# Kernel tuning notes

Hardware: AMD Instinct MI355X
Metric: run time of the kernel (lower is better)

Reference implementation:

```python
import jax, jax.numpy as jnp
import numpy as np

THRESHOLDS = (0.3, 0.4, 0.5)
EPS_NORM = 1e-12   # F.normalize eps
EPS_MAX = 1e-5     # added to max before rescale


def setup_inputs() -> dict:
    key = jax.random.key(0)
    k1, k2 = jax.random.split(key)
    cam = jax.random.uniform(k1, (4, 64, 64), dtype=jnp.float32)
    feat = jax.random.normal(k2, (4, 256, 64, 64), dtype=jnp.float32)
    return {"cam": cam, "feat": feat}


def reference(cam, feat):
    # multi-threshold soft mask: mean of hard masks at each threshold -> (B,1,H,W)
    masks = jnp.stack([(cam >= t).astype(feat.dtype) for t in THRESHOLDS], axis=1)
    m = masks.mean(axis=1)[:, None]  # (B,1,H,W)
    masked = feat * m  # (B,C,H,W)

    B, C, H, W = masked.shape
    f = masked.reshape(B, C, H * W)  # (B,C,N)
    # L2-normalize over channel dim (torch F.normalize, dim=1)
    norm = jnp.sqrt(jnp.sum(f * f, axis=1, keepdims=True))
    fn = f / jnp.maximum(norm, EPS_NORM)

    # full pairwise similarity (B,N,N), then CAM-weighted aggregation
    sim = jnp.einsum('bcn,bcm->bnm', fn, fn)      # (B,N,N)
    camf = cam.reshape(B, H * W)                  # (B,N)
    out = jnp.einsum('bnm,bm->bn', sim, camf)     # (B,N)

    mn = out.min(axis=1, keepdims=True)
    mx = out.max(axis=1, keepdims=True) + EPS_MAX
    ref = ((out - mn) / (mx - mn)).reshape(B, H, W)

    loss = jnp.mean(jnp.abs(ref - jax.lax.stop_gradient(cam)))
    return ref, loss
```

## Files before the change

### kernel.cpp

```cpp
#include <hip/hip_runtime.h>


constexpr int B  = 4;
constexpr int C  = 256;
constexpr int N  = 4096;
constexpr int BN = B * N;
constexpr int CN = C * N;
constexpr int NBLK1 = 512;

__device__ __forceinline__ float wsum(float v) {
#pragma unroll
    for (int o = 32; o > 0; o >>= 1) v += __shfl_down(v, o, 64);
    return v;
}
__device__ __forceinline__ float wmin64(float v) {
#pragma unroll
    for (int o = 32; o > 0; o >>= 1) v = fminf(v, __shfl_down(v, o, 64));
    return v;
}
__device__ __forceinline__ float wmax64(float v) {
#pragma unroll
    for (int o = 32; o > 0; o >>= 1) v = fmaxf(v, __shfl_down(v, o, 64));
    return v;
}

__global__ void __launch_bounds__(256) k_norm_vpart(
    const float* __restrict__ cam, const float* __restrict__ feat,
    float* __restrict__ s, float* __restrict__ v_part,
    unsigned int* __restrict__ cnt)
{
    if (blockIdx.x == 0 && threadIdx.x == 0) *cnt = 0u;
    const int t   = threadIdx.x;
    const int pix = t & 31;
    const int g   = t >> 5;
    const int bk  = blockIdx.x;
    const int b   = bk >> 7;
    const int n0  = (bk * 32) & (N - 1);

    __shared__ float red[8][33];
    __shared__ float w_sh[32];

    {
        const float* fp = feat + (size_t)b * CN + (size_t)(g * 32) * N + n0 + pix;
        float ss = 0.f;
#pragma unroll 8
        for (int cc = 0; cc < 32; ++cc) {
            float x = fp[(size_t)cc * N];
            ss = fmaf(x, x, ss);
        }
        red[g][pix] = ss;
    }
    __syncthreads();
    if (t < 32) {
        float tot = 0.f;
#pragma unroll
        for (int gg = 0; gg < 8; ++gg) tot += red[gg][t];
        float cv = cam[bk * 32 + t];
        float m  = ((cv >= 0.3f ? 1.f : 0.f) + (cv >= 0.4f ? 1.f : 0.f) +
                    (cv >= 0.5f ? 1.f : 0.f)) * (1.f / 3.f);
        float norm = m * sqrtf(tot);
        float sc = m / fmaxf(norm, 1e-12f);
        s[bk * 32 + t] = sc;
        w_sh[t] = sc * cv;
    }
    __syncthreads();

    {
        const float* fp = feat + (size_t)b * CN + (size_t)t * N + n0;
        float acc = 0.f;
#pragma unroll
        for (int pp = 0; pp < 8; ++pp) {
            float4 x = *(const float4*)(fp + pp * 4);
            acc = fmaf(x.x, w_sh[pp * 4 + 0], acc);
            acc = fmaf(x.y, w_sh[pp * 4 + 1], acc);
            acc = fmaf(x.z, w_sh[pp * 4 + 2], acc);
            acc = fmaf(x.w, w_sh[pp * 4 + 3], acc);
        }
        v_part[bk * 256 + t] = acc;
    }
}

__global__ void __launch_bounds__(256) k_vreduce(
    const float* __restrict__ v_part, float* __restrict__ v)
{
    const int c = threadIdx.x;
    const int b = blockIdx.x;
    const float* base = v_part + (size_t)b * 128 * 256 + c;
    float acc = 0.f;
#pragma unroll 8
    for (int k = 0; k < 128; ++k) acc += base[k * 256];
    v[b * 256 + c] = acc;
}

__global__ void __launch_bounds__(256) k_out(
    const float* __restrict__ feat, const float* __restrict__ s,
    const float* __restrict__ v, float* __restrict__ ob,
    float* __restrict__ bmn, float* __restrict__ bmx)
{
    const int t   = threadIdx.x;
    const int pix = t & 31;
    const int g   = t >> 5;
    const int bk  = blockIdx.x;
    const int b   = bk >> 7;
    const int n0  = (bk * 32) & (N - 1);

    __shared__ float vs[C];
    vs[t] = v[b * C + t];
    __syncthreads();

    const float* fp = feat + (size_t)b * CN + (size_t)(g * 32) * N + n0 + pix;
    float acc = 0.f;
#pragma unroll 8
    for (int cc = 0; cc < 32; ++cc)
        acc = fmaf(fp[(size_t)cc * N], vs[g * 32 + cc], acc);

    __shared__ float red[8][33];
    red[g][pix] = acc;
    __syncthreads();
    if (t < 32) {
        float tot = 0.f;
#pragma unroll
        for (int gg = 0; gg < 8; ++gg) tot += red[gg][t];
        float o = s[bk * 32 + t] * tot;
        ob[bk * 32 + t] = o;
        float mn = o, mx = o;
#pragma unroll
        for (int o2 = 16; o2 > 0; o2 >>= 1) {
            mn = fminf(mn, __shfl_down(mn, o2, 64));
            mx = fmaxf(mx, __shfl_down(mx, o2, 64));
        }
        if (t == 0) { bmn[bk] = mn; bmx[bk] = mx; }
    }
}

__global__ void __launch_bounds__(256) k_final(
    const float* __restrict__ ob, const float* __restrict__ cam,
    const float* __restrict__ bmn, const float* __restrict__ bmx,
    float* __restrict__ out, float* __restrict__ part, unsigned int* __restrict__ cnt)
{
    const int t = threadIdx.x, blk = blockIdx.x;
    const int p = blk * 256 + t;
    const int b = blk >> 4;

    __shared__ float sh[2];
    if (t < 64) {
        float a = fminf(bmn[b * 128 + t], bmn[b * 128 + 64 + t]);
        a = wmin64(a);
        if (t == 0) sh[0] = a;
    } else if (t < 128) {
        int l = t - 64;
        float a = fmaxf(bmx[b * 128 + l], bmx[b * 128 + 64 + l]);
        a = wmax64(a);
        if (l == 0) sh[1] = a;
    }
    __syncthreads();
    const float mn = sh[0];
    const float mx = sh[1] + 1e-5f;

    float r = (ob[p] - mn) / (mx - mn);
    out[p] = r;
    float ad = fabsf(r - cam[p]);

    __shared__ float red[4];
    float ps = wsum(ad);
    if ((t & 63) == 0) red[t >> 6] = ps;
    __syncthreads();

    __shared__ int lastflag;
    if (t == 0) {
        float tot = (red[0] + red[1]) + (red[2] + red[3]);
        __hip_atomic_store(&part[blk], tot, __ATOMIC_RELEASE, __HIP_MEMORY_SCOPE_AGENT);
        unsigned old = __hip_atomic_fetch_add(cnt, 1u, __ATOMIC_ACQ_REL,
                                              __HIP_MEMORY_SCOPE_AGENT);
        lastflag = (old == 63u) ? 1 : 0;
    }
    __syncthreads();
    if (lastflag && t < 64) {
        float x = __hip_atomic_load(&part[t], __ATOMIC_ACQUIRE,
                                    __HIP_MEMORY_SCOPE_AGENT);
        x = wsum(x);
        if (t == 0) out[BN] = x * (1.f / (float)BN);
    }
}

extern "C" void kernel_launch(void* const* d_in, const int* in_sizes, int n_in,
                              void* d_out, int out_size, void* d_ws, size_t ws_size,
                              hipStream_t stream) {
    const float* cam  = (const float*)d_in[0];
    const float* feat = (const float*)d_in[1];
    float* out = (float*)d_out;
    float* ws  = (float*)d_ws;

    float* s      = ws;
    float* v_part = ws + 16384;
    float* v      = ws + 147456;
    float* ob     = ws + 148480;
    float* bmn    = ws + 164864;
    float* bmx    = ws + 165376;
    float* part   = ws + 165888;
    unsigned int* cnt = (unsigned int*)(ws + 165952);

    k_norm_vpart<<<NBLK1, 256, 0, stream>>>(cam, feat, s, v_part, cnt);
    k_vreduce   <<<B,     256, 0, stream>>>(v_part, v);
    k_out       <<<NBLK1, 256, 0, stream>>>(feat, s, v, ob, bmn, bmx);
    k_final     <<<64,    256, 0, stream>>>(ob, cam, bmn, bmx, out, part, cnt);
}
```

Baseline: 23.06 us.

## Cache feature tile in LDS and fuse final normalization into last output block

The first kernel now stages the 256x32 feature tile in shared memory while computing norms, so the weighted channel sum reads LDS instead of reloading feat from global memory. The separate final kernel is removed. The last block of the output kernel, detected via an atomic counter, performs the min/max rescale and loss reduction over all 16K pixels. This saves one launch and one global pass, but serialises the final step onto a single block and uses about 33KB of LDS per block, which may lower occupancy.

```diff
diff --git a/kernel.cpp b/kernel.cpp
--- a/kernel.cpp
+++ b/kernel.cpp
@@ -6,7 +6,7 @@
 constexpr int N  = 4096;
 constexpr int BN = B * N;
 constexpr int CN = C * N;
-constexpr int NBLK1 = 512;
+constexpr int NBLK = 512;
 
 __device__ __forceinline__ float wsum(float v) {
 #pragma unroll
@@ -30,6 +30,11 @@
     unsigned int* __restrict__ cnt)
 {
     if (blockIdx.x == 0 && threadIdx.x == 0) *cnt = 0u;
+
+    __shared__ float tile[C * 33];
+    __shared__ float red[8][33];
+    __shared__ float w_sh[32];
+
     const int t   = threadIdx.x;
     const int pix = t & 31;
     const int g   = t >> 5;
@@ -37,16 +42,14 @@
     const int b   = bk >> 7;
     const int n0  = (bk * 32) & (N - 1);
 
-    __shared__ float red[8][33];
-    __shared__ float w_sh[32];
-
     {
         const float* fp = feat + (size_t)b * CN + (size_t)(g * 32) * N + n0 + pix;
         float ss = 0.f;
-#pragma unroll 8
+#pragma unroll
         for (int cc = 0; cc < 32; ++cc) {
             float x = fp[(size_t)cc * N];
             ss = fmaf(x, x, ss);
+            tile[(g * 32 + cc) * 33 + pix] = x;
         }
         red[g][pix] = ss;
     }
@@ -58,24 +61,17 @@
         float cv = cam[bk * 32 + t];
         float m  = ((cv >= 0.3f ? 1.f : 0.f) + (cv >= 0.4f ? 1.f : 0.f) +
                     (cv >= 0.5f ? 1.f : 0.f)) * (1.f / 3.f);
-        float norm = m * sqrtf(tot);
-        float sc = m / fmaxf(norm, 1e-12f);
+        float sc = m / fmaxf(m * sqrtf(tot), 1e-12f);
         s[bk * 32 + t] = sc;
         w_sh[t] = sc * cv;
     }
     __syncthreads();
 
     {
-        const float* fp = feat + (size_t)b * CN + (size_t)t * N + n0;
         float acc = 0.f;
 #pragma unroll
-        for (int pp = 0; pp < 8; ++pp) {
-            float4 x = *(const float4*)(fp + pp * 4);
-            acc = fmaf(x.x, w_sh[pp * 4 + 0], acc);
-            acc = fmaf(x.y, w_sh[pp * 4 + 1], acc);
-            acc = fmaf(x.z, w_sh[pp * 4 + 2], acc);
-            acc = fmaf(x.w, w_sh[pp * 4 + 3], acc);
-        }
+        for (int pp = 0; pp < 32; ++pp)
+            acc = fmaf(tile[t * 33 + pp], w_sh[pp], acc);
         v_part[bk * 256 + t] = acc;
     }
 }
@@ -92,10 +88,11 @@
     v[b * 256 + c] = acc;
 }
 
-__global__ void __launch_bounds__(256) k_out(
+__global__ void __launch_bounds__(256) k_out_final(
     const float* __restrict__ feat, const float* __restrict__ s,
-    const float* __restrict__ v, float* __restrict__ ob,
-    float* __restrict__ bmn, float* __restrict__ bmx)
+    const float* __restrict__ v, const float* __restrict__ cam,
+    float* __restrict__ ob, float* __restrict__ bmn, float* __restrict__ bmx,
+    float* __restrict__ out, unsigned int* __restrict__ cnt)
 {
     const int t   = threadIdx.x;
     const int pix = t & 31;
@@ -131,56 +128,46 @@
         }
         if (t == 0) { bmn[bk] = mn; bmx[bk] = mx; }
     }
-}
 
-__global__ void __launch_bounds__(256) k_final(
-    const float* __restrict__ ob, const float* __restrict__ cam,
-    const float* __restrict__ bmn, const float* __restrict__ bmx,
-    float* __restrict__ out, float* __restrict__ part, unsigned int* __restrict__ cnt)
-{
-    const int t = threadIdx.x, blk = blockIdx.x;
-    const int p = blk * 256 + t;
-    const int b = blk >> 4;
-
-    __shared__ float sh[2];
-    if (t < 64) {
-        float a = fminf(bmn[b * 128 + t], bmn[b * 128 + 64 + t]);
-        a = wmin64(a);
-        if (t == 0) sh[0] = a;
-    } else if (t < 128) {
-        int l = t - 64;
-        float a = fmaxf(bmx[b * 128 + l], bmx[b * 128 + 64 + l]);
-        a = wmax64(a);
-        if (l == 0) sh[1] = a;
+    __shared__ int lastflag;
+    __syncthreads();
+    if (t == 0) {
+        __threadfence();
+        unsigned old = __hip_atomic_fetch_add(cnt, 1u, __ATOMIC_ACQ_REL,
+                                              __HIP_MEMORY_SCOPE_AGENT);
+        lastflag = (old == NBLK - 1u) ? 1 : 0;
     }
     __syncthreads();
-    const float mn = sh[0];
-    const float mx = sh[1] + 1e-5f;
+    if (!lastflag) return;
 
-    float r = (ob[p] - mn) / (mx - mn);
-    out[p] = r;
-    float ad = fabsf(r - cam[p]);
-
-    __shared__ float red[4];
-    float ps = wsum(ad);
-    if ((t & 63) == 0) red[t >> 6] = ps;
+    __shared__ float shmn[4], shmx[4];
+    {
+        const int bb = t >> 6, l = t & 63;
+        float a = fminf(bmn[bb * 128 + l], bmn[bb * 128 + 64 + l]);
+        a = wmin64(a);
+        float z = fmaxf(bmx[bb * 128 + l], bmx[bb * 128 + 64 + l]);
+        z = wmax64(z);
+        if (l == 0) { shmn[bb] = a; shmx[bb] = z; }
+    }
     __syncthreads();
 
-    __shared__ int lastflag;
-    if (t == 0) {
-        float tot = (red[0] + red[1]) + (red[2] + red[3]);
-        __hip_atomic_store(&part[blk], tot, __ATOMIC_RELEASE, __HIP_MEMORY_SCOPE_AGENT);
-        unsigned old = __hip_atomic_fetch_add(cnt, 1u, __ATOMIC_ACQ_REL,
-                                              __HIP_MEMORY_SCOPE_AGENT);
-        lastflag = (old == 63u) ? 1 : 0;
+    float lsum = 0.f;
+#pragma unroll 4
+    for (int i = 0; i < 64; ++i) {
+        int p = i * 256 + t;
+        int bb = i >> 4;
+        float mn  = shmn[bb];
+        float mxa = shmx[bb] + 1e-5f;
+        float r = (ob[p] - mn) / (mxa - mn);
+        out[p] = r;
+        lsum += fabsf(r - cam[p]);
     }
+    __shared__ float red2[4];
+    float ps = wsum(lsum);
+    if ((t & 63) == 0) red2[t >> 6] = ps;
     __syncthreads();
-    if (lastflag && t < 64) {
-        float x = __hip_atomic_load(&part[t], __ATOMIC_ACQUIRE,
-                                    __HIP_MEMORY_SCOPE_AGENT);
-        x = wsum(x);
-        if (t == 0) out[BN] = x * (1.f / (float)BN);
-    }
+    if (t == 0)
+        out[BN] = ((red2[0] + red2[1]) + (red2[2] + red2[3])) * (1.f / (float)BN);
 }
 
 extern "C" void kernel_launch(void* const* d_in, const int* in_sizes, int n_in,
@@ -197,11 +184,9 @@
     float* ob     = ws + 148480;
     float* bmn    = ws + 164864;
     float* bmx    = ws + 165376;
-    float* part   = ws + 165888;
-    unsigned int* cnt = (unsigned int*)(ws + 165952);
+    unsigned int* cnt = (unsigned int*)(ws + 165888);
 
-    k_norm_vpart<<<NBLK1, 256, 0, stream>>>(cam, feat, s, v_part, cnt);
-    k_vreduce   <<<B,     256, 0, stream>>>(v_part, v);
-    k_out       <<<NBLK1, 256, 0, stream>>>(feat, s, v, ob, bmn, bmx);
-    k_final     <<<64,    256, 0, stream>>>(ob, cam, bmn, bmx, out, part, cnt);
+    k_norm_vpart<<<NBLK, 256, 0, stream>>>(cam, feat, s, v_part, cnt);
+    k_vreduce   <<<B,    256, 0, stream>>>(v_part, v);
+    k_out_final <<<NBLK, 256, 0, stream>>>(feat, s, v, cam, ob, bmn, bmx, out, cnt);
 }
```

Result: slower. 50.62 us (+119.5%).
